# Performance work log

Measured on AMD Instinct MI355X. Metric: run time of the kernel, lower is better.

The kernel has to match this reference:

```python
import jax, jax.numpy as jnp
import numpy as np

NX = 1024
N_HEAD = 16
HEAD_DIM = NX // N_HEAD


def setup_inputs() -> dict:
    key = jax.random.key(0)
    k1, k2, k3 = jax.random.split(key, 3)
    x = jax.random.normal(k1, (4, 2048, NX), dtype=jnp.float32)
    attention_mask = jnp.zeros((4, 1, 1, 2048), dtype=jnp.float32)
    c_attn_w = jax.random.truncated_normal(k2, -2.0, 2.0, (NX, 3 * NX), dtype=jnp.float32) * 0.02
    c_attn_b = jnp.zeros((3 * NX,), dtype=jnp.float32)
    c_proj_w = jax.random.truncated_normal(k3, -2.0, 2.0, (NX, NX), dtype=jnp.float32) * 0.02
    c_proj_b = jnp.zeros((NX,), dtype=jnp.float32)
    return {"x": x, "attention_mask": attention_mask,
            "c_attn_w": c_attn_w, "c_attn_b": c_attn_b,
            "c_proj_w": c_proj_w, "c_proj_b": c_proj_b}


def _split_heads(t):
    # (B, S, NX) -> (B, H, S, D)
    B, S, _ = t.shape
    return t.reshape(B, S, N_HEAD, HEAD_DIM).transpose(0, 2, 1, 3)


def reference(x, attention_mask, c_attn_w, c_attn_b, c_proj_w, c_proj_b):
    # fused QKV projection (TFConv1D == dense)
    qkv = x @ c_attn_w + c_attn_b  # (B, S, 3*NX)
    query, key, value = jnp.split(qkv, 3, axis=2)
    q = _split_heads(query)  # (B, H, S, D)
    k = _split_heads(key)
    v = _split_heads(value)
    # full score matrix (naive attention, matches original)
    w = jnp.einsum('bhqd,bhkd->bhqk', q, k)
    w = w / jnp.sqrt(jnp.asarray(HEAD_DIM, dtype=w.dtype))  # scale=True
    w = w + attention_mask  # additive mask, broadcast (B,1,1,S)
    w = jax.nn.softmax(w + 1e-9, axis=-1)  # stable_softmax
    # dropout is identity at eval; head_mask is None
    a = jnp.einsum('bhqk,bhkd->bhqd', w, v)
    # merge heads: (B, H, S, D) -> (B, S, NX)
    B, H, S, D = a.shape
    a = a.transpose(0, 2, 1, 3).reshape(B, S, H * D)
    out = a @ c_proj_w + c_proj_b
    return out
```

## Files before the change

kernel.cpp:

```cpp
#include <hip/hip_runtime.h>
#include <hip/hip_bf16.h>
#include <cstdint>
#include <cstddef>

#define SLEN 2048
#define NHEAD 16
#define HDIM 64

typedef short bf16x8 __attribute__((ext_vector_type(8)));
typedef float f32x4 __attribute__((ext_vector_type(4)));

__device__ __forceinline__ unsigned short f2bf(float f) {
  union { __hip_bfloat16 b; unsigned short u; } cv;
  cv.b = __float2bfloat16(f);
  return cv.u;
}

__device__ __forceinline__ unsigned pack2bf(float a, float b) {
  return (unsigned)f2bf(a) | ((unsigned)f2bf(b) << 16);
}

__device__ __forceinline__ void async16(unsigned short* lds, const unsigned short* g) {
  __builtin_amdgcn_global_load_lds(
      (const __attribute__((address_space(1))) unsigned int*)g,
      (__attribute__((address_space(3))) unsigned int*)lds, 16, 0, 0);
}

__global__ __launch_bounds__(256) void cvt_bf16(
    const float* __restrict__ in, unsigned short* __restrict__ out, int n8)
{
  int i = blockIdx.x * 256 + threadIdx.x;
  if (i >= n8) return;
  const float4 a = *(const float4*)(in + (size_t)i*8);
  const float4 b = *(const float4*)(in + (size_t)i*8 + 4);
  ushort4 o0 = {f2bf(a.x), f2bf(a.y), f2bf(a.z), f2bf(a.w)};
  ushort4 o1 = {f2bf(b.x), f2bf(b.y), f2bf(b.z), f2bf(b.w)};
  *(ushort4*)(out + (size_t)i*8)     = o0;
  *(ushort4*)(out + (size_t)i*8 + 4) = o1;
}

__global__ __launch_bounds__(256) void scale_mask(
    const float* __restrict__ in, float* __restrict__ out, int n)
{
  int i = blockIdx.x * 256 + threadIdx.x;
  if (i < n) out[i] = in[i] * 1.44269504088896f;
}

__global__ __launch_bounds__(256) void transpose_w(
    const float* __restrict__ W, unsigned short* __restrict__ Wt, int K, int N)
{
  __shared__ unsigned short T[32][36];
  const int kb = blockIdx.y * 32, nb = blockIdx.x * 32;
  const int r = threadIdx.x >> 3, c4 = (threadIdx.x & 7) * 4;
  float4 w = *(const float4*)(W + (size_t)(kb + r)*N + nb + c4);
  T[c4+0][r] = f2bf(w.x); T[c4+1][r] = f2bf(w.y);
  T[c4+2][r] = f2bf(w.z); T[c4+3][r] = f2bf(w.w);
  __syncthreads();
  ushort4 o = {T[r][c4], T[r][c4+1], T[r][c4+2], T[r][c4+3]};
  *(ushort4*)(Wt + (size_t)(nb + r)*K + kb + c4) = o;
}

__global__ __launch_bounds__(256, 2) void gemm1_mfma(
    const unsigned short* __restrict__ Xb,
    const unsigned short* __restrict__ Wt,
    const float* __restrict__ Bias,
    unsigned short* __restrict__ Qb, unsigned short* __restrict__ Kb,
    unsigned short* __restrict__ Vt, int m0)
{
  __shared__ union {
    struct { unsigned short A[128*32]; unsigned short B[128*32]; } s;
    unsigned short vt[128*136];
  } u;
  const int tid = threadIdx.x;
  const int wid = tid >> 6, lane = tid & 63;
  const int lo = lane & 15, hi = lane >> 4;
  const int wr = wid >> 1, wc = wid & 1;
  const int mtile = blockIdx.y * 128;
  const int nbase = blockIdx.x * 128;

  f32x4 acc[4][4];
  #pragma unroll
  for (int i = 0; i < 4; i++)
    #pragma unroll
    for (int j = 0; j < 4; j++) { f32x4 z = {0.f,0.f,0.f,0.f}; acc[i][j] = z; }

  const int ldrow = 32*wid + (lane >> 2);
  const int koff  = (lane & 3) * 8;

  const unsigned short* Abase = Xb + (size_t)(m0 + mtile)*1024;
  const unsigned short* Bbase = Wt + (size_t)nbase*1024;

  for (int k0 = 0; k0 < 1024; k0 += 32) {
    __syncthreads();
    #pragma unroll
    for (int cc = 0; cc < 2; cc++) {
      int r = ldrow + cc*16;
      async16(&u.s.A[r*32 + koff], Abase + (size_t)r*1024 + k0 + koff);
      async16(&u.s.B[r*32 + koff], Bbase + (size_t)r*1024 + k0 + koff);
    }
    __syncthreads();
    bf16x8 af[4], bf[4];
    #pragma unroll
    for (int mi = 0; mi < 4; mi++)
      af[mi] = *(const bf16x8*)&u.s.A[(wr*64 + mi*16 + lo)*32 + hi*8];
    #pragma unroll
    for (int ni = 0; ni < 4; ni++)
      bf[ni] = *(const bf16x8*)&u.s.B[(wc*64 + ni*16 + lo)*32 + hi*8];
    #pragma unroll
    for (int mi = 0; mi < 4; mi++)
      #pragma unroll
      for (int ni = 0; ni < 4; ni++)
        acc[mi][ni] = __builtin_amdgcn_mfma_f32_16x16x32_bf16(
            af[mi], bf[ni], acc[mi][ni], 0, 0, 0);
  }

  float bias_[4];
  #pragma unroll
  for (int ni = 0; ni < 4; ni++) bias_[ni] = Bias[nbase + wc*64 + ni*16 + lo];

  const int bl = mtile >> 11;
  const int s0 = mtile & 2047;

  if (nbase < 2048) {
    unsigned short* dst = (nbase < 1024) ? Qb : Kb;
    const int nb2 = nbase & 1023;
    #pragma unroll
    for (int mi = 0; mi < 4; mi++)
      #pragma unroll
      for (int i = 0; i < 4; i++) {
        int s = s0 + wr*64 + mi*16 + hi*4 + i;
        #pragma unroll
        for (int ni = 0; ni < 4; ni++) {
          int n = nb2 + wc*64 + ni*16 + lo;
          int h = n >> 6, d = n & 63;
          dst[((size_t)(bl*16 + h)*SLEN + s)*HDIM + d] =
              f2bf(acc[mi][ni][i] + bias_[ni]);
        }
      }
  } else {
    __syncthreads();
    #pragma unroll
    for (int mi = 0; mi < 4; mi++)
      #pragma unroll
      for (int ni = 0; ni < 4; ni++)
        #pragma unroll
        for (int i = 0; i < 4; i++) {
          int ml = wr*64 + mi*16 + hi*4 + i;
          int nl = wc*64 + ni*16 + lo;
          u.vt[nl*136 + ml] = f2bf(acc[mi][ni][i] + bias_[ni]);
        }
    __syncthreads();
    const int rv = tid >> 1, halfc = (tid & 1)*64;
    const int ng = nbase - 2048 + rv;
    const int h = ng >> 6, d = ng & 63;
    unsigned short* drow = Vt + ((size_t)(bl*16 + h)*HDIM + d)*SLEN + s0 + halfc;
    #pragma unroll
    for (int j = 0; j < 8; j++) {
      bf16x8 v = *(const bf16x8*)&u.vt[rv*136 + halfc + j*8];
      *(bf16x8*)(drow + j*8) = v;
    }
  }
}

__global__ __launch_bounds__(256, 4) void attn_mfma(
    const unsigned short* __restrict__ Qb, const unsigned short* __restrict__ Kb,
    const unsigned short* __restrict__ Vt, const float* __restrict__ maskL,
    unsigned short* __restrict__ O, int b0)
{
  __shared__ unsigned short Ks[2][64*64];
  __shared__ unsigned short Vs[2][64*64];
  __shared__ unsigned short Ps[4][16][64];

  const int tid = threadIdx.x;
  const int wid = tid >> 6, lane = tid & 63;
  const int lo = lane & 15, hi = lane >> 4;
  const int qt = blockIdx.x & 31;
  const int bh = blockIdx.x >> 5;
  const int bglob = b0 + (bh >> 4);
  const float* mrow = maskL + (size_t)bglob * SLEN;

  const unsigned short* qg = Qb + ((size_t)bh*SLEN + qt*64)*HDIM;
  const unsigned short* kg = Kb + (size_t)bh*SLEN*HDIM;
  const unsigned short* vg = Vt + (size_t)bh*HDIM*SLEN;

  const unsigned short* qrow = qg + (size_t)(wid*16 + lo)*HDIM;
  const bf16x8 qa0 = *(const bf16x8*)(qrow + hi*8);
  const bf16x8 qa1 = *(const bf16x8*)(qrow + 32 + hi*8);

  auto STAGE = [&](int bu, int kt2) {
    #pragma unroll
    for (int i = 0; i < 2; i++) {
      int slot = tid + i*256;
      int row = slot >> 3, p = slot & 7;
      int c = p ^ (row & 7);
      async16(&Ks[bu][row*64 + p*8], kg + (size_t)(kt2*64 + row)*HDIM + c*8);
      async16(&Vs[bu][row*64 + p*8], vg + (size_t)row*SLEN + kt2*64 + c*8);
    }
  };

  float m_ = -INFINITY, l_ = 0.f;
  f32x4 oacc[4];
  #pragma unroll
  for (int i = 0; i < 4; i++) { f32x4 z = {0.f,0.f,0.f,0.f}; oacc[i] = z; }

  const float SC2 = 0.125f * 1.44269504088896f;
  const int x7 = lo & 7;
  const int pswz = (lo & 7) << 3;

  STAGE(0, 0);
  for (int kt = 0; kt < SLEN/64; kt++) {
    const int cur = kt & 1;
    __syncthreads();
    if (kt + 1 < SLEN/64) STAGE(cur ^ 1, kt + 1);

    f32x4 sacc[4];
    __builtin_amdgcn_s_setprio(1);
    #pragma unroll
    for (int blk = 0; blk < 4; blk++) {
      const int row = blk*16 + lo;
      bf16x8 kb0 = *(const bf16x8*)&Ks[cur][row*64 + ((hi     ^ x7)*8)];
      bf16x8 kb1 = *(const bf16x8*)&Ks[cur][row*64 + (((hi+4) ^ x7)*8)];
      f32x4 z = {0.f,0.f,0.f,0.f};
      z = __builtin_amdgcn_mfma_f32_16x16x32_bf16(kb0, qa0, z, 0, 0, 0);
      sacc[blk] = __builtin_amdgcn_mfma_f32_16x16x32_bf16(kb1, qa1, z, 0, 0, 0);
    }
    __builtin_amdgcn_s_setprio(0);

    float sl[4][4];
    float rmax = -INFINITY;
    #pragma unroll
    for (int blk = 0; blk < 4; blk++) {
      float4 mk = *(const float4*)(mrow + kt*64 + blk*16 + hi*4);
      sl[blk][0] = fmaf(sacc[blk][0], SC2, mk.x);
      sl[blk][1] = fmaf(sacc[blk][1], SC2, mk.y);
      sl[blk][2] = fmaf(sacc[blk][2], SC2, mk.z);
      sl[blk][3] = fmaf(sacc[blk][3], SC2, mk.w);
      #pragma unroll
      for (int i = 0; i < 4; i++) rmax = fmaxf(rmax, sl[blk][i]);
    }
    rmax = fmaxf(rmax, __shfl_xor(rmax, 16));
    rmax = fmaxf(rmax, __shfl_xor(rmax, 32));

    if (!__all(rmax <= m_ + 8.f)) {
      float mnew = fmaxf(m_, rmax);
      float corr = exp2f(m_ - mnew);
      m_ = mnew;
      l_ *= corr;
      float c4[4];
      #pragma unroll
      for (int i = 0; i < 4; i++) c4[i] = __shfl(corr, hi*4 + i);
      #pragma unroll
      for (int dblk = 0; dblk < 4; dblk++)
        #pragma unroll
        for (int i = 0; i < 4; i++) oacc[dblk][i] *= c4[i];
    }

    float psum = 0.f;
    #pragma unroll
    for (int blk = 0; blk < 4; blk++) {
      #pragma unroll
      for (int t = 0; t < 2; t++) {
        float p0 = exp2f(sl[blk][2*t]   - m_);
        float p1 = exp2f(sl[blk][2*t+1] - m_);
        psum += p0 + p1;
        *(unsigned*)&Ps[wid][lo][(blk*16 + hi*4 + 2*t) ^ pswz] = pack2bf(p0, p1);
      }
    }
    psum += __shfl_xor(psum, 16);
    psum += __shfl_xor(psum, 32);
    l_ += psum;

    bf16x8 pa0 = *(const bf16x8*)&Ps[wid][lo][(hi*8)      ^ pswz];
    bf16x8 pa1 = *(const bf16x8*)&Ps[wid][lo][(32 + hi*8) ^ pswz];
    __builtin_amdgcn_s_setprio(1);
    #pragma unroll
    for (int dblk = 0; dblk < 4; dblk++) {
      const int row = dblk*16 + lo;
      bf16x8 vb0 = *(const bf16x8*)&Vs[cur][row*64 + ((hi     ^ x7)*8)];
      bf16x8 vb1 = *(const bf16x8*)&Vs[cur][row*64 + (((hi+4) ^ x7)*8)];
      oacc[dblk] = __builtin_amdgcn_mfma_f32_16x16x32_bf16(pa0, vb0, oacc[dblk], 0, 0, 0);
      oacc[dblk] = __builtin_amdgcn_mfma_f32_16x16x32_bf16(pa1, vb1, oacc[dblk], 0, 0, 0);
    }
    __builtin_amdgcn_s_setprio(0);
  }

  float invl = 1.f / l_;
  float inv4[4];
  #pragma unroll
  for (int i = 0; i < 4; i++) inv4[i] = __shfl(invl, hi*4 + i);

  const size_t obase = ((size_t)bh*SLEN + qt*64 + wid*16)*HDIM;
  #pragma unroll
  for (int i = 0; i < 4; i++) {
    int row = hi*4 + i;
    #pragma unroll
    for (int dblk = 0; dblk < 4; dblk++)
      O[obase + (size_t)row*HDIM + dblk*16 + lo] = f2bf(oacc[dblk][i]*inv4[i]);
  }
}

__global__ __launch_bounds__(256, 2) void gemm2_mfma(
    const unsigned short* __restrict__ Ob,
    const unsigned short* __restrict__ Wt,
    const float* __restrict__ Bias,
    float* __restrict__ Out, int m0)
{
  __shared__ unsigned short As[128*32];
  __shared__ unsigned short Bs[128*32];
  const int tid = threadIdx.x;
  const int wid = tid >> 6, lane = tid & 63;
  const int lo = lane & 15, hi = lane >> 4;
  const int wr = wid >> 1, wc = wid & 1;
  const int mtile = blockIdx.y * 128;
  const int nbase = blockIdx.x * 128;

  f32x4 acc[4][4];
  #pragma unroll
  for (int i = 0; i < 4; i++)
    #pragma unroll
    for (int j = 0; j < 4; j++) { f32x4 z = {0.f,0.f,0.f,0.f}; acc[i][j] = z; }

  const int ldrow = 32*wid + (lane >> 2);
  const int koff  = (lane & 3) * 8;

  const int bl = mtile >> 11;
  const int s0 = mtile & 2047;
  const unsigned short* Bbase = Wt + (size_t)nbase*1024;

  for (int k0 = 0; k0 < 1024; k0 += 32) {
    const int h = k0 >> 6;
    const int dpart = (k0 & 63) + koff;
    __syncthreads();
    #pragma unroll
    for (int cc = 0; cc < 2; cc++) {
      int r = ldrow + cc*16;
      const unsigned short* ga =
          Ob + ((size_t)(bl*16 + h)*SLEN + s0 + r)*HDIM + dpart;
      async16(&As[r*32 + koff], ga);
      async16(&Bs[r*32 + koff], Bbase + (size_t)r*1024 + k0 + koff);
    }
    __syncthreads();
    bf16x8 af[4], bf[4];
    #pragma unroll
    for (int mi = 0; mi < 4; mi++)
      af[mi] = *(const bf16x8*)&As[(wr*64 + mi*16 + lo)*32 + hi*8];
    #pragma unroll
    for (int ni = 0; ni < 4; ni++)
      bf[ni] = *(const bf16x8*)&Bs[(wc*64 + ni*16 + lo)*32 + hi*8];
    #pragma unroll
    for (int mi = 0; mi < 4; mi++)
      #pragma unroll
      for (int ni = 0; ni < 4; ni++)
        acc[mi][ni] = __builtin_amdgcn_mfma_f32_16x16x32_bf16(
            af[mi], bf[ni], acc[mi][ni], 0, 0, 0);
  }

  float bias_[4];
  #pragma unroll
  for (int ni = 0; ni < 4; ni++) bias_[ni] = Bias[nbase + wc*64 + ni*16 + lo];

  #pragma unroll
  for (int mi = 0; mi < 4; mi++)
    #pragma unroll
    for (int i = 0; i < 4; i++) {
      int m = m0 + mtile + wr*64 + mi*16 + hi*4 + i;
      float* orow = Out + (size_t)m*1024 + nbase + wc*64 + lo;
      #pragma unroll
      for (int ni = 0; ni < 4; ni++)
        orow[ni*16] = acc[mi][ni][i] + bias_[ni];
    }
}

extern "C" void kernel_launch(void* const* d_in, const int* in_sizes, int n_in,
                              void* d_out, int out_size, void* d_ws, size_t ws_size,
                              hipStream_t stream) {
  const float* x     = (const float*)d_in[0];
  const float* amask = (const float*)d_in[1];
  const float* wat   = (const float*)d_in[2];
  const float* bat   = (const float*)d_in[3];
  const float* wpr   = (const float*)d_in[4];
  const float* bpr   = (const float*)d_in[5];
  float* out = (float*)d_out;

  unsigned short* WattnT = (unsigned short*)d_ws;
  unsigned short* WprojT = WattnT + (size_t)3072*1024;
  unsigned short* xb     = WprojT + (size_t)1024*1024;
  float*          maskL  = (float*)(xb + (size_t)8192*1024);
  unsigned short* chunk0 = (unsigned short*)(maskL + 4*SLEN);

  const size_t PB = (size_t)NHEAD * SLEN * HDIM;
  const size_t base_bytes = ((size_t)3072*1024 + (size_t)1024*1024 + (size_t)8192*1024) * 2
                          + (size_t)4*SLEN*4;
  int bc = 1;
  if (ws_size >= base_bytes + 4 * 4 * PB * 2)      bc = 4;
  else if (ws_size >= base_bytes + 2 * 4 * PB * 2) bc = 2;

  cvt_bf16<<<dim3((8192*1024/8 + 255)/256), dim3(256), 0, stream>>>(
      x, xb, 8192*1024/8);
  scale_mask<<<dim3((4*SLEN + 255)/256), dim3(256), 0, stream>>>(
      amask, maskL, 4*SLEN);
  transpose_w<<<dim3(3072/32, 1024/32), dim3(256), 0, stream>>>(wat, WattnT, 1024, 3072);
  transpose_w<<<dim3(1024/32, 1024/32), dim3(256), 0, stream>>>(wpr, WprojT, 1024, 1024);

  for (int b0 = 0; b0 < 4; b0 += bc) {
    unsigned short* Qb = chunk0;
    unsigned short* Kb = Qb + (size_t)bc * PB;
    unsigned short* Vt = Kb + (size_t)bc * PB;
    unsigned short* Ob = Vt + (size_t)bc * PB;
    int Mrows = bc * SLEN;
    gemm1_mfma<<<dim3(24, Mrows/128), dim3(256), 0, stream>>>(
        xb, WattnT, bat, Qb, Kb, Vt, b0 * SLEN);
    attn_mfma<<<dim3(bc * NHEAD * (SLEN/64)), dim3(256), 0, stream>>>(
        Qb, Kb, Vt, maskL, Ob, b0);
    gemm2_mfma<<<dim3(8, Mrows/128), dim3(256), 0, stream>>>(
        Ob, WprojT, bpr, out, b0 * SLEN);
  }
}
```

Measured before the change: 266.8 us.

## Process two 64-row query groups per attention block and sum rows via MFMA

Each attention block now handles 128 query rows (two groups of 64) instead of 64, so every staged K/V tile in LDS serves twice as many queries and global K/V traffic is halved. The grid shrinks by half to match. The softmax row sum is now computed by an MFMA against a ones vector instead of shuffle reductions. In exchange, registers per thread roughly double for accumulators, which may reduce occupancy under the launch bound of 4. Fewer blocks also means less parallelism per launch. The row sum now uses the bf16-rounded probabilities, which changes numerics slightly.

```diff
diff --git a/kernel.cpp b/kernel.cpp
--- a/kernel.cpp
+++ b/kernel.cpp
@@ -174,18 +174,22 @@
   const int tid = threadIdx.x;
   const int wid = tid >> 6, lane = tid & 63;
   const int lo = lane & 15, hi = lane >> 4;
-  const int qt = blockIdx.x & 31;
-  const int bh = blockIdx.x >> 5;
+  const int qt = blockIdx.x & 15;
+  const int bh = blockIdx.x >> 4;
   const int bglob = b0 + (bh >> 4);
   const float* mrow = maskL + (size_t)bglob * SLEN;
 
-  const unsigned short* qg = Qb + ((size_t)bh*SLEN + qt*64)*HDIM;
+  const unsigned short* qg = Qb + ((size_t)bh*SLEN + qt*128)*HDIM;
   const unsigned short* kg = Kb + (size_t)bh*SLEN*HDIM;
   const unsigned short* vg = Vt + (size_t)bh*HDIM*SLEN;
 
-  const unsigned short* qrow = qg + (size_t)(wid*16 + lo)*HDIM;
-  const bf16x8 qa0 = *(const bf16x8*)(qrow + hi*8);
-  const bf16x8 qa1 = *(const bf16x8*)(qrow + 32 + hi*8);
+  bf16x8 qa[2][2];
+  #pragma unroll
+  for (int g = 0; g < 2; g++) {
+    const unsigned short* qrow = qg + (size_t)(g*64 + wid*16 + lo)*HDIM;
+    qa[g][0] = *(const bf16x8*)(qrow + hi*8);
+    qa[g][1] = *(const bf16x8*)(qrow + 32 + hi*8);
+  }
 
   auto STAGE = [&](int bu, int kt2) {
     #pragma unroll
@@ -198,11 +202,18 @@
     }
   };
 
-  float m_ = -INFINITY, l_ = 0.f;
-  f32x4 oacc[4];
-  #pragma unroll
-  for (int i = 0; i < 4; i++) { f32x4 z = {0.f,0.f,0.f,0.f}; oacc[i] = z; }
-
+  float m_[2] = {-INFINITY, -INFINITY};
+  f32x4 lacc[2];
+  f32x4 oacc[2][4];
+  #pragma unroll
+  for (int g = 0; g < 2; g++) {
+    f32x4 z = {0.f,0.f,0.f,0.f};
+    lacc[g] = z;
+    #pragma unroll
+    for (int i = 0; i < 4; i++) oacc[g][i] = z;
+  }
+
+  const bf16x8 ones = {0x3F80,0x3F80,0x3F80,0x3F80,0x3F80,0x3F80,0x3F80,0x3F80};
   const float SC2 = 0.125f * 1.44269504088896f;
   const int x7 = lo & 7;
   const int pswz = (lo & 7) << 3;
@@ -213,89 +224,94 @@
     __syncthreads();
     if (kt + 1 < SLEN/64) STAGE(cur ^ 1, kt + 1);
 
-    f32x4 sacc[4];
-    __builtin_amdgcn_s_setprio(1);
-    #pragma unroll
-    for (int blk = 0; blk < 4; blk++) {
-      const int row = blk*16 + lo;
-      bf16x8 kb0 = *(const bf16x8*)&Ks[cur][row*64 + ((hi     ^ x7)*8)];
-      bf16x8 kb1 = *(const bf16x8*)&Ks[cur][row*64 + (((hi+4) ^ x7)*8)];
-      f32x4 z = {0.f,0.f,0.f,0.f};
-      z = __builtin_amdgcn_mfma_f32_16x16x32_bf16(kb0, qa0, z, 0, 0, 0);
-      sacc[blk] = __builtin_amdgcn_mfma_f32_16x16x32_bf16(kb1, qa1, z, 0, 0, 0);
-    }
-    __builtin_amdgcn_s_setprio(0);
-
-    float sl[4][4];
-    float rmax = -INFINITY;
-    #pragma unroll
-    for (int blk = 0; blk < 4; blk++) {
-      float4 mk = *(const float4*)(mrow + kt*64 + blk*16 + hi*4);
-      sl[blk][0] = fmaf(sacc[blk][0], SC2, mk.x);
-      sl[blk][1] = fmaf(sacc[blk][1], SC2, mk.y);
-      sl[blk][2] = fmaf(sacc[blk][2], SC2, mk.z);
-      sl[blk][3] = fmaf(sacc[blk][3], SC2, mk.w);
-      #pragma unroll
-      for (int i = 0; i < 4; i++) rmax = fmaxf(rmax, sl[blk][i]);
-    }
-    rmax = fmaxf(rmax, __shfl_xor(rmax, 16));
-    rmax = fmaxf(rmax, __shfl_xor(rmax, 32));
-
-    if (!__all(rmax <= m_ + 8.f)) {
-      float mnew = fmaxf(m_, rmax);
-      float corr = exp2f(m_ - mnew);
-      m_ = mnew;
-      l_ *= corr;
-      float c4[4];
-      #pragma unroll
-      for (int i = 0; i < 4; i++) c4[i] = __shfl(corr, hi*4 + i);
+    #pragma unroll
+    for (int g = 0; g < 2; g++) {
+      f32x4 sacc[4];
+      __builtin_amdgcn_s_setprio(1);
+      #pragma unroll
+      for (int blk = 0; blk < 4; blk++) {
+        const int row = blk*16 + lo;
+        bf16x8 kb0 = *(const bf16x8*)&Ks[cur][row*64 + ((hi     ^ x7)*8)];
+        bf16x8 kb1 = *(const bf16x8*)&Ks[cur][row*64 + (((hi+4) ^ x7)*8)];
+        f32x4 z = {0.f,0.f,0.f,0.f};
+        z = __builtin_amdgcn_mfma_f32_16x16x32_bf16(kb0, qa[g][0], z, 0, 0, 0);
+        sacc[blk] = __builtin_amdgcn_mfma_f32_16x16x32_bf16(kb1, qa[g][1], z, 0, 0, 0);
+      }
+      __builtin_amdgcn_s_setprio(0);
+
+      #pragma unroll
+      for (int blk = 0; blk < 4; blk++) {
+        float4 mk = *(const float4*)(mrow + kt*64 + blk*16 + hi*4);
+        sacc[blk][0] = fmaf(sacc[blk][0], SC2, mk.x);
+        sacc[blk][1] = fmaf(sacc[blk][1], SC2, mk.y);
+        sacc[blk][2] = fmaf(sacc[blk][2], SC2, mk.z);
+        sacc[blk][3] = fmaf(sacc[blk][3], SC2, mk.w);
+      }
+      float t0 = fmaxf(fmaxf(sacc[0][0], sacc[0][1]), sacc[0][2]);
+      float t1 = fmaxf(fmaxf(sacc[0][3], sacc[1][0]), sacc[1][1]);
+      float t2 = fmaxf(fmaxf(sacc[1][2], sacc[1][3]), sacc[2][0]);
+      float t3 = fmaxf(fmaxf(sacc[2][1], sacc[2][2]), sacc[2][3]);
+      float t4 = fmaxf(fmaxf(sacc[3][0], sacc[3][1]), sacc[3][2]);
+      float rmax = fmaxf(fmaxf(fmaxf(t0, t1), t2),
+                         fmaxf(fmaxf(t3, t4), sacc[3][3]));
+      rmax = fmaxf(rmax, __shfl_xor(rmax, 16));
+      rmax = fmaxf(rmax, __shfl_xor(rmax, 32));
+
+      if (!__all(rmax <= m_[g] + 8.f)) {
+        float mnew = fmaxf(m_[g], rmax);
+        float corr = exp2f(m_[g] - mnew);
+        m_[g] = mnew;
+        float c4[4];
+        #pragma unroll
+        for (int i = 0; i < 4; i++) c4[i] = __shfl(corr, hi*4 + i);
+        #pragma unroll
+        for (int i = 0; i < 4; i++) lacc[g][i] *= c4[i];
+        #pragma unroll
+        for (int dblk = 0; dblk < 4; dblk++)
+          #pragma unroll
+          for (int i = 0; i < 4; i++) oacc[g][dblk][i] *= c4[i];
+      }
+
+      #pragma unroll
+      for (int blk = 0; blk < 4; blk++) {
+        #pragma unroll
+        for (int t = 0; t < 2; t++) {
+          float p0 = exp2f(sacc[blk][2*t]   - m_[g]);
+          float p1 = exp2f(sacc[blk][2*t+1] - m_[g]);
+          *(unsigned*)&Ps[wid][lo][(blk*16 + hi*4 + 2*t) ^ pswz] = pack2bf(p0, p1);
+        }
+      }
+
+      bf16x8 pa0 = *(const bf16x8*)&Ps[wid][lo][(hi*8)      ^ pswz];
+      bf16x8 pa1 = *(const bf16x8*)&Ps[wid][lo][(32 + hi*8) ^ pswz];
+
+      lacc[g] = __builtin_amdgcn_mfma_f32_16x16x32_bf16(pa0, ones, lacc[g], 0, 0, 0);
+      lacc[g] = __builtin_amdgcn_mfma_f32_16x16x32_bf16(pa1, ones, lacc[g], 0, 0, 0);
+
+      __builtin_amdgcn_s_setprio(1);
+      #pragma unroll
+      for (int dblk = 0; dblk < 4; dblk++) {
+        const int row = dblk*16 + lo;
+        bf16x8 vb0 = *(const bf16x8*)&Vs[cur][row*64 + ((hi     ^ x7)*8)];
+        bf16x8 vb1 = *(const bf16x8*)&Vs[cur][row*64 + (((hi+4) ^ x7)*8)];
+        oacc[g][dblk] = __builtin_amdgcn_mfma_f32_16x16x32_bf16(pa0, vb0, oacc[g][dblk], 0, 0, 0);
+        oacc[g][dblk] = __builtin_amdgcn_mfma_f32_16x16x32_bf16(pa1, vb1, oacc[g][dblk], 0, 0, 0);
+      }
+      __builtin_amdgcn_s_setprio(0);
+    }
+  }
+
+  #pragma unroll
+  for (int g = 0; g < 2; g++) {
+    const size_t obase = ((size_t)bh*SLEN + qt*128 + g*64 + wid*16)*HDIM;
+    #pragma unroll
+    for (int i = 0; i < 4; i++) {
+      float inv = 1.f / lacc[g][i];
+      int row = hi*4 + i;
       #pragma unroll
       for (int dblk = 0; dblk < 4; dblk++)
-        #pragma unroll
-        for (int i = 0; i < 4; i++) oacc[dblk][i] *= c4[i];
-    }
-
-    float psum = 0.f;
-    #pragma unroll
-    for (int blk = 0; blk < 4; blk++) {
-      #pragma unroll
-      for (int t = 0; t < 2; t++) {
-        float p0 = exp2f(sl[blk][2*t]   - m_);
-        float p1 = exp2f(sl[blk][2*t+1] - m_);
-        psum += p0 + p1;
-        *(unsigned*)&Ps[wid][lo][(blk*16 + hi*4 + 2*t) ^ pswz] = pack2bf(p0, p1);
-      }
-    }
-    psum += __shfl_xor(psum, 16);
-    psum += __shfl_xor(psum, 32);
-    l_ += psum;
-
-    bf16x8 pa0 = *(const bf16x8*)&Ps[wid][lo][(hi*8)      ^ pswz];
-    bf16x8 pa1 = *(const bf16x8*)&Ps[wid][lo][(32 + hi*8) ^ pswz];
-    __builtin_amdgcn_s_setprio(1);
-    #pragma unroll
-    for (int dblk = 0; dblk < 4; dblk++) {
-      const int row = dblk*16 + lo;
-      bf16x8 vb0 = *(const bf16x8*)&Vs[cur][row*64 + ((hi     ^ x7)*8)];
-      bf16x8 vb1 = *(const bf16x8*)&Vs[cur][row*64 + (((hi+4) ^ x7)*8)];
-      oacc[dblk] = __builtin_amdgcn_mfma_f32_16x16x32_bf16(pa0, vb0, oacc[dblk], 0, 0, 0);
-      oacc[dblk] = __builtin_amdgcn_mfma_f32_16x16x32_bf16(pa1, vb1, oacc[dblk], 0, 0, 0);
-    }
-    __builtin_amdgcn_s_setprio(0);
-  }
-
-  float invl = 1.f / l_;
-  float inv4[4];
-  #pragma unroll
-  for (int i = 0; i < 4; i++) inv4[i] = __shfl(invl, hi*4 + i);
-
-  const size_t obase = ((size_t)bh*SLEN + qt*64 + wid*16)*HDIM;
-  #pragma unroll
-  for (int i = 0; i < 4; i++) {
-    int row = hi*4 + i;
-    #pragma unroll
-    for (int dblk = 0; dblk < 4; dblk++)
-      O[obase + (size_t)row*HDIM + dblk*16 + lo] = f2bf(oacc[dblk][i]*inv4[i]);
+        O[obase + (size_t)row*HDIM + dblk*16 + lo] = f2bf(oacc[g][dblk][i]*inv);
+    }
   }
 }
 
@@ -410,7 +426,7 @@
     int Mrows = bc * SLEN;
     gemm1_mfma<<<dim3(24, Mrows/128), dim3(256), 0, stream>>>(
         xb, WattnT, bat, Qb, Kb, Vt, b0 * SLEN);
-    attn_mfma<<<dim3(bc * NHEAD * (SLEN/64)), dim3(256), 0, stream>>>(
+    attn_mfma<<<dim3(bc * NHEAD * (SLEN/128)), dim3(256), 0, stream>>>(
         Qb, Kb, Vt, maskL, Ob, b0);
     gemm2_mfma<<<dim3(8, Mrows/128), dim3(256), 0, stream>>>(
         Ob, WprojT, bpr, out, b0 * SLEN);
```

Measured after the change: 263.6 us. Within noise of the previous version (-1.2%).

## Restructure attention kernel to 8-wave 128-query blocks with 32-key tiles

Applied to the files above, without the earlier changes.

The attention kernel now uses 512-thread blocks covering 128 query rows, so each staged K/V tile is shared by twice as many waves. The key tile shrinks from 64 to 32, which halves LDS per block and lets the K and V loads be split across the two halves of the block. The row-sum of probabilities is computed by an MFMA against a ones vector, replacing the shuffle reductions. A block-index swizzle spreads blocks across XCDs. The costs are twice as many loop iterations and barriers, more synchronisation per block, and a higher launch-bounds occupancy target that may limit registers per thread.

```diff
diff --git a/kernel.cpp b/kernel.cpp
--- a/kernel.cpp
+++ b/kernel.cpp
@@ -162,24 +162,27 @@
   }
 }
 
-__global__ __launch_bounds__(256, 4) void attn_mfma(
+__global__ __launch_bounds__(512, 8) void attn_mfma(
     const unsigned short* __restrict__ Qb, const unsigned short* __restrict__ Kb,
     const unsigned short* __restrict__ Vt, const float* __restrict__ maskL,
     unsigned short* __restrict__ O, int b0)
 {
-  __shared__ unsigned short Ks[2][64*64];
-  __shared__ unsigned short Vs[2][64*64];
-  __shared__ unsigned short Ps[4][16][64];
+  __shared__ unsigned short Ks[2][32*64];
+  __shared__ unsigned short Vs[2][64*32];
+  __shared__ unsigned short Ps[8][16][40];
 
   const int tid = threadIdx.x;
   const int wid = tid >> 6, lane = tid & 63;
   const int lo = lane & 15, hi = lane >> 4;
-  const int qt = blockIdx.x & 31;
-  const int bh = blockIdx.x >> 5;
+
+  const int nwg = gridDim.x;
+  const int swz = (blockIdx.x & 7) * (nwg >> 3) + (blockIdx.x >> 3);
+  const int qt = swz & 15;
+  const int bh = swz >> 4;
   const int bglob = b0 + (bh >> 4);
   const float* mrow = maskL + (size_t)bglob * SLEN;
 
-  const unsigned short* qg = Qb + ((size_t)bh*SLEN + qt*64)*HDIM;
+  const unsigned short* qg = Qb + ((size_t)bh*SLEN + qt*128)*HDIM;
   const unsigned short* kg = Kb + (size_t)bh*SLEN*HDIM;
   const unsigned short* vg = Vt + (size_t)bh*HDIM*SLEN;
 
@@ -188,35 +191,37 @@
   const bf16x8 qa1 = *(const bf16x8*)(qrow + 32 + hi*8);
 
   auto STAGE = [&](int bu, int kt2) {
-    #pragma unroll
-    for (int i = 0; i < 2; i++) {
-      int slot = tid + i*256;
-      int row = slot >> 3, p = slot & 7;
-      int c = p ^ (row & 7);
-      async16(&Ks[bu][row*64 + p*8], kg + (size_t)(kt2*64 + row)*HDIM + c*8);
-      async16(&Vs[bu][row*64 + p*8], vg + (size_t)row*SLEN + kt2*64 + c*8);
+    if (tid < 256) {
+      int row = tid >> 3, p = tid & 7, c = p ^ (row & 7);
+      async16(&Ks[bu][row*64 + p*8], kg + (size_t)(kt2*32 + row)*HDIM + c*8);
+    } else {
+      int t = tid - 256;
+      int row = t >> 2, p = t & 3, c = p ^ (row & 3);
+      async16(&Vs[bu][row*32 + p*8], vg + (size_t)row*SLEN + kt2*32 + c*8);
     }
   };
 
-  float m_ = -INFINITY, l_ = 0.f;
+  float m_ = -INFINITY;
+  f32x4 lacc = {0.f,0.f,0.f,0.f};
   f32x4 oacc[4];
   #pragma unroll
   for (int i = 0; i < 4; i++) { f32x4 z = {0.f,0.f,0.f,0.f}; oacc[i] = z; }
 
+  const bf16x8 ones = {0x3F80,0x3F80,0x3F80,0x3F80,0x3F80,0x3F80,0x3F80,0x3F80};
   const float SC2 = 0.125f * 1.44269504088896f;
   const int x7 = lo & 7;
-  const int pswz = (lo & 7) << 3;
+  const int x3 = lo & 3;
 
   STAGE(0, 0);
-  for (int kt = 0; kt < SLEN/64; kt++) {
+  for (int kt = 0; kt < SLEN/32; kt++) {
     const int cur = kt & 1;
     __syncthreads();
-    if (kt + 1 < SLEN/64) STAGE(cur ^ 1, kt + 1);
-
-    f32x4 sacc[4];
+    if (kt + 1 < SLEN/32) STAGE(cur ^ 1, kt + 1);
+
+    f32x4 sacc[2];
     __builtin_amdgcn_s_setprio(1);
     #pragma unroll
-    for (int blk = 0; blk < 4; blk++) {
+    for (int blk = 0; blk < 2; blk++) {
       const int row = blk*16 + lo;
       bf16x8 kb0 = *(const bf16x8*)&Ks[cur][row*64 + ((hi     ^ x7)*8)];
       bf16x8 kb1 = *(const bf16x8*)&Ks[cur][row*64 + (((hi+4) ^ x7)*8)];
@@ -226,18 +231,18 @@
     }
     __builtin_amdgcn_s_setprio(0);
 
-    float sl[4][4];
-    float rmax = -INFINITY;
-    #pragma unroll
-    for (int blk = 0; blk < 4; blk++) {
-      float4 mk = *(const float4*)(mrow + kt*64 + blk*16 + hi*4);
-      sl[blk][0] = fmaf(sacc[blk][0], SC2, mk.x);
-      sl[blk][1] = fmaf(sacc[blk][1], SC2, mk.y);
-      sl[blk][2] = fmaf(sacc[blk][2], SC2, mk.z);
-      sl[blk][3] = fmaf(sacc[blk][3], SC2, mk.w);
-      #pragma unroll
-      for (int i = 0; i < 4; i++) rmax = fmaxf(rmax, sl[blk][i]);
-    }
+    #pragma unroll
+    for (int blk = 0; blk < 2; blk++) {
+      float4 mk = *(const float4*)(mrow + kt*32 + blk*16 + hi*4);
+      sacc[blk][0] = fmaf(sacc[blk][0], SC2, mk.x);
+      sacc[blk][1] = fmaf(sacc[blk][1], SC2, mk.y);
+      sacc[blk][2] = fmaf(sacc[blk][2], SC2, mk.z);
+      sacc[blk][3] = fmaf(sacc[blk][3], SC2, mk.w);
+    }
+    float t0 = fmaxf(fmaxf(sacc[0][0], sacc[0][1]), sacc[0][2]);
+    float t1 = fmaxf(fmaxf(sacc[0][3], sacc[1][0]), sacc[1][1]);
+    float t2 = fmaxf(fmaxf(sacc[1][2], sacc[1][3]), t0);
+    float rmax = fmaxf(t1, t2);
     rmax = fmaxf(rmax, __shfl_xor(rmax, 16));
     rmax = fmaxf(rmax, __shfl_xor(rmax, 32));
 
@@ -245,57 +250,49 @@
       float mnew = fmaxf(m_, rmax);
       float corr = exp2f(m_ - mnew);
       m_ = mnew;
-      l_ *= corr;
       float c4[4];
       #pragma unroll
       for (int i = 0; i < 4; i++) c4[i] = __shfl(corr, hi*4 + i);
+      #pragma unroll
+      for (int i = 0; i < 4; i++) lacc[i] *= c4[i];
       #pragma unroll
       for (int dblk = 0; dblk < 4; dblk++)
         #pragma unroll
         for (int i = 0; i < 4; i++) oacc[dblk][i] *= c4[i];
     }
 
-    float psum = 0.f;
-    #pragma unroll
-    for (int blk = 0; blk < 4; blk++) {
-      #pragma unroll
-      for (int t = 0; t < 2; t++) {
-        float p0 = exp2f(sl[blk][2*t]   - m_);
-        float p1 = exp2f(sl[blk][2*t+1] - m_);
-        psum += p0 + p1;
-        *(unsigned*)&Ps[wid][lo][(blk*16 + hi*4 + 2*t) ^ pswz] = pack2bf(p0, p1);
-      }
-    }
-    psum += __shfl_xor(psum, 16);
-    psum += __shfl_xor(psum, 32);
-    l_ += psum;
-
-    bf16x8 pa0 = *(const bf16x8*)&Ps[wid][lo][(hi*8)      ^ pswz];
-    bf16x8 pa1 = *(const bf16x8*)&Ps[wid][lo][(32 + hi*8) ^ pswz];
+    #pragma unroll
+    for (int blk = 0; blk < 2; blk++) {
+      float p0 = exp2f(sacc[blk][0] - m_);
+      float p1 = exp2f(sacc[blk][1] - m_);
+      float p2 = exp2f(sacc[blk][2] - m_);
+      float p3 = exp2f(sacc[blk][3] - m_);
+      uint2 w = {pack2bf(p0, p1), pack2bf(p2, p3)};
+      *(uint2*)&Ps[wid][lo][blk*16 + hi*4] = w;
+    }
+
+    bf16x8 pa = *(const bf16x8*)&Ps[wid][lo][hi*8];
+
+    lacc = __builtin_amdgcn_mfma_f32_16x16x32_bf16(pa, ones, lacc, 0, 0, 0);
+
     __builtin_amdgcn_s_setprio(1);
     #pragma unroll
     for (int dblk = 0; dblk < 4; dblk++) {
       const int row = dblk*16 + lo;
-      bf16x8 vb0 = *(const bf16x8*)&Vs[cur][row*64 + ((hi     ^ x7)*8)];
-      bf16x8 vb1 = *(const bf16x8*)&Vs[cur][row*64 + (((hi+4) ^ x7)*8)];
-      oacc[dblk] = __builtin_amdgcn_mfma_f32_16x16x32_bf16(pa0, vb0, oacc[dblk], 0, 0, 0);
-      oacc[dblk] = __builtin_amdgcn_mfma_f32_16x16x32_bf16(pa1, vb1, oacc[dblk], 0, 0, 0);
+      bf16x8 vb = *(const bf16x8*)&Vs[cur][row*32 + ((hi ^ x3)*8)];
+      oacc[dblk] = __builtin_amdgcn_mfma_f32_16x16x32_bf16(pa, vb, oacc[dblk], 0, 0, 0);
     }
     __builtin_amdgcn_s_setprio(0);
   }
 
-  float invl = 1.f / l_;
-  float inv4[4];
-  #pragma unroll
-  for (int i = 0; i < 4; i++) inv4[i] = __shfl(invl, hi*4 + i);
-
-  const size_t obase = ((size_t)bh*SLEN + qt*64 + wid*16)*HDIM;
+  const size_t obase = ((size_t)bh*SLEN + qt*128 + wid*16)*HDIM;
   #pragma unroll
   for (int i = 0; i < 4; i++) {
+    float inv = 1.f / lacc[i];
     int row = hi*4 + i;
     #pragma unroll
     for (int dblk = 0; dblk < 4; dblk++)
-      O[obase + (size_t)row*HDIM + dblk*16 + lo] = f2bf(oacc[dblk][i]*inv4[i]);
+      O[obase + (size_t)row*HDIM + dblk*16 + lo] = f2bf(oacc[dblk][i]*inv);
   }
 }
 
@@ -410,7 +407,7 @@
     int Mrows = bc * SLEN;
     gemm1_mfma<<<dim3(24, Mrows/128), dim3(256), 0, stream>>>(
         xb, WattnT, bat, Qb, Kb, Vt, b0 * SLEN);
-    attn_mfma<<<dim3(bc * NHEAD * (SLEN/64)), dim3(256), 0, stream>>>(
+    attn_mfma<<<dim3(bc * NHEAD * (SLEN/128)), dim3(512), 0, stream>>>(
         Qb, Kb, Vt, maskL, Ob, b0);
     gemm2_mfma<<<dim3(8, Mrows/128), dim3(256), 0, stream>>>(
         Ob, WprojT, bpr, out, b0 * SLEN);
```

New measurement: 456.6 us. 71.1% more time.
